# Kernel tuning notes

Hardware: AMD Instinct MI355X
Metric: run time of the kernel (lower is better)

## Reference

```python
import jax, jax.numpy as jnp
import numpy as np

DIM = 512
HEADS = 8
HEAD_DIM = 64
INNER = HEADS * HEAD_DIM  # 512
FF = DIM * 2
EPS = 1e-5


def layernorm(x, g, b):
    mu = jnp.mean(x, axis=-1, keepdims=True)
    var = jnp.var(x, axis=-1, keepdims=True)
    return (x - mu) * jax.lax.rsqrt(var + EPS) * g + b


def setup_inputs() -> dict:
    key = jax.random.key(0)
    ks = jax.random.split(key, 10)
    s = lambda fan_in: 1.0 / np.sqrt(fan_in)
    return {
        "x": jax.random.normal(ks[0], (4, 2048, DIM), dtype=jnp.float32),
        "ln1_g": jnp.ones((DIM,), jnp.float32),
        "ln1_b": jnp.zeros((DIM,), jnp.float32),
        "w_qkv": jax.random.normal(ks[1], (DIM, 3 * INNER), jnp.float32) * s(DIM),
        "w_out": jax.random.normal(ks[2], (INNER, DIM), jnp.float32) * s(INNER),
        "b_out": jnp.zeros((DIM,), jnp.float32),
        "ln2_g": jnp.ones((DIM,), jnp.float32),
        "ln2_b": jnp.zeros((DIM,), jnp.float32),
        "w1": jax.random.normal(ks[3], (DIM, FF), jnp.float32) * s(DIM),
        "b1": jnp.zeros((FF,), jnp.float32),
        "w2": jax.random.normal(ks[4], (FF, DIM), jnp.float32) * s(FF),
        "b2": jnp.zeros((DIM,), jnp.float32),
    }


def reference(x, ln1_g, ln1_b, w_qkv, w_out, b_out, ln2_g, ln2_b, w1, b1, w2, b2):
    b, n, _ = x.shape
    # --- pre-LN MHSA ---
    h = layernorm(x, ln1_g, ln1_b)
    qkv = h @ w_qkv  # [b, n, 3*inner]
    q, k, v = jnp.split(qkv, 3, axis=-1)
    to_heads = lambda t: t.reshape(b, n, HEADS, HEAD_DIM).transpose(0, 2, 1, 3)
    q, k, v = to_heads(q), to_heads(k), to_heads(v)
    scores = jnp.einsum('bhid,bhjd->bhij', q, k) * (HEAD_DIM ** -0.5)
    attn = jax.nn.softmax(scores, axis=-1)
    attended = jnp.einsum('bhij,bhjd->bhid', attn, v)
    attended = attended.transpose(0, 2, 1, 3).reshape(b, n, INNER)
    x = attended @ w_out + b_out + x
    # --- pre-LN MLP ---
    h = layernorm(x, ln2_g, ln2_b)
    h = jax.nn.gelu(h @ w1 + b1, approximate=False)
    x = h @ w2 + b2 + x
    return x
```

## Files before the change

kernel.cpp:

```cpp
#include <hip/hip_runtime.h>
#include <math.h>


#define TOKENS 8192
#define SEQ    2048
typedef unsigned short u16;
typedef __attribute__((ext_vector_type(8))) _Float16 h8;
typedef __attribute__((ext_vector_type(4))) float f32x4;
typedef __attribute__((ext_vector_type(4))) unsigned short u16x4;

#define BAR_V0 asm volatile("s_waitcnt vmcnt(0) lgkmcnt(0)\n\ts_barrier" ::: "memory")
#define BAR_V4 asm volatile("s_waitcnt vmcnt(4) lgkmcnt(0)\n\ts_barrier" ::: "memory")

__device__ __forceinline__ u16 f2h(float f) {
    _Float16 h = (_Float16)f;
    return __builtin_bit_cast(u16, h);
}
__device__ __forceinline__ void a16(void* lds, const void* g) {
    __builtin_amdgcn_global_load_lds(
        (const __attribute__((address_space(1))) unsigned int*)g,
        (__attribute__((address_space(3))) unsigned int*)lds, 16, 0, 0);
}
__device__ __forceinline__ float gelu_exact(float v) {
    return 0.5f * v * (1.0f + erff(v * 0.70710678118654752f));
}

__global__ __launch_bounds__(256) void prep_k(const float* __restrict__ wqkv,
                                              const float* __restrict__ wout,
                                              const float* __restrict__ w1,
                                              const float* __restrict__ w2,
                                              u16* __restrict__ dqkv,
                                              u16* __restrict__ dout,
                                              u16* __restrict__ d1,
                                              u16* __restrict__ d2,
                                              const float* __restrict__ x,
                                              const float* __restrict__ g,
                                              const float* __restrict__ bta,
                                              u16* __restrict__ oh) {
    const int tid = threadIdx.x;
    if (blockIdx.x >= 512) {
        const int lane = tid & 63;
        const int row  = ((blockIdx.x - 512) << 2) + (tid >> 6);
        const float* xr = x + ((size_t)row << 9) + (lane << 3);
        float v[8];
        *(float4*)&v[0] = *(const float4*)xr;
        *(float4*)&v[4] = *(const float4*)(xr + 4);
        float s = 0.f, ss = 0.f;
#pragma unroll
        for (int i = 0; i < 8; i++) { s += v[i]; ss += v[i] * v[i]; }
#pragma unroll
        for (int m = 32; m; m >>= 1) {
            s  += __shfl_xor(s, m, 64);
            ss += __shfl_xor(ss, m, 64);
        }
        const float mu   = s * (1.0f / 512.0f);
        const float rstd = rsqrtf(ss * (1.0f / 512.0f) - mu * mu + 1e-5f);
        float gg[8], bb[8];
        *(float4*)&gg[0] = *(const float4*)(g + (lane << 3));
        *(float4*)&gg[4] = *(const float4*)(g + (lane << 3) + 4);
        *(float4*)&bb[0] = *(const float4*)(bta + (lane << 3));
        *(float4*)&bb[4] = *(const float4*)(bta + (lane << 3) + 4);
        union { u16 us[8]; uint4 q; } H;
#pragma unroll
        for (int i = 0; i < 8; i++) H.us[i] = f2h((v[i] - mu) * rstd * gg[i] + bb[i]);
        *(uint4*)&oh[((size_t)row << 9) + (lane << 3)] = H.q;
        return;
    }
    __shared__ float t[64][65];
    int b = blockIdx.x;
    const float* src; u16* dst; int K, N, n0, k0;
    if (b < 192)      { src = wqkv; dst = dqkv; K = 512;  N = 1536; n0 = (b % 24) << 6; k0 = (b / 24) << 6; }
    else if (b < 256) { b -= 192; src = wout; dst = dout; K = 512;  N = 512;  n0 = (b & 7) << 6;  k0 = (b >> 3) << 6; }
    else if (b < 384) { b -= 256; src = w1;   dst = d1;   K = 512;  N = 1024; n0 = (b & 15) << 6; k0 = (b >> 4) << 6; }
    else              { b -= 384; src = w2;   dst = d2;   K = 1024; N = 512;  n0 = (b & 7) << 6;  k0 = (b >> 3) << 6; }
    {
        const int kr = tid >> 2, nc = (tid & 3) << 4;
        const float* p = src + (size_t)(k0 + kr) * N + n0 + nc;
#pragma unroll
        for (int i = 0; i < 4; i++)
            *(float4*)&t[kr][nc + (i << 2)] = *(const float4*)(p + (i << 2));
    }
    __syncthreads();
    {
        const int nr = tid >> 2, kc = (tid & 3) << 4;
        union { u16 us[16]; uint4 q[2]; } H;
#pragma unroll
        for (int i = 0; i < 16; i++) H.us[i] = f2h(t[kc + i][nr]);
        const size_t o = (size_t)(n0 + nr) * K + k0 + kc;
        *(uint4*)&dst[o] = H.q[0];
        *(uint4*)&dst[o + 8] = H.q[1];
    }
}

__global__ __launch_bounds__(256) void ln_k(const float* __restrict__ x,
                                            const float* __restrict__ g,
                                            const float* __restrict__ bta,
                                            u16* __restrict__ oh) {
    const int lane = threadIdx.x & 63;
    const int row  = (blockIdx.x << 2) + (threadIdx.x >> 6);
    const float* xr = x + ((size_t)row << 9) + (lane << 3);
    float v[8];
    *(float4*)&v[0] = *(const float4*)xr;
    *(float4*)&v[4] = *(const float4*)(xr + 4);
    float s = 0.f, ss = 0.f;
#pragma unroll
    for (int i = 0; i < 8; i++) { s += v[i]; ss += v[i] * v[i]; }
#pragma unroll
    for (int m = 32; m; m >>= 1) {
        s  += __shfl_xor(s, m, 64);
        ss += __shfl_xor(ss, m, 64);
    }
    const float mu   = s * (1.0f / 512.0f);
    const float rstd = rsqrtf(ss * (1.0f / 512.0f) - mu * mu + 1e-5f);
    float gg[8], bb[8];
    *(float4*)&gg[0] = *(const float4*)(g + (lane << 3));
    *(float4*)&gg[4] = *(const float4*)(g + (lane << 3) + 4);
    *(float4*)&bb[0] = *(const float4*)(bta + (lane << 3));
    *(float4*)&bb[4] = *(const float4*)(bta + (lane << 3) + 4);
    union { u16 us[8]; uint4 q; } H;
#pragma unroll
    for (int i = 0; i < 8; i++) H.us[i] = f2h((v[i] - mu) * rstd * gg[i] + bb[i]);
    *(uint4*)&oh[((size_t)row << 9) + (lane << 3)] = H.q;
}

template <int EPI>
__global__ __launch_bounds__(256, 3) void sgemm_k(
    const u16* __restrict__ A, const u16* __restrict__ B,
    const float* __restrict__ bias, const float* __restrict__ res,
    float* __restrict__ Cf, u16* __restrict__ Ch, u16* __restrict__ Dh,
    int M, int N, int K) {
    __shared__ u16 sm[16384];
    const int tid = threadIdx.x;
    const int lane = tid & 63, wv = tid >> 6;
    const int col = lane & 15, quad = lane >> 4;
    const int wm = (wv & 1) << 6, wn = (wv >> 1) << 6;
    const int bm = blockIdx.y << 7, bn = blockIdx.x << 7;

    const int r0 = tid >> 2,         c0 = (tid & 3) ^ ((r0 >> 1) & 3);
    const int r1 = (tid + 256) >> 2, c1 = (tid & 3) ^ ((r1 >> 1) & 3);
    const u16* Ag0 = A + (size_t)(bm + r0) * K + c0 * 8;
    const u16* Ag1 = A + (size_t)(bm + r1) * K + c1 * 8;
    const u16* Bg0 = B + (size_t)(bn + r0) * K + c0 * 8;
    const u16* Bg1 = B + (size_t)(bn + r1) * K + c1 * 8;
    const int lw0 = wv * 512, lw1 = wv * 512 + 2048;
    const int swz = (col >> 1) & 3;
    const f32x4 z4 = {0.f, 0.f, 0.f, 0.f};
    f32x4 acc[4][4] = {{z4,z4,z4,z4},{z4,z4,z4,z4},{z4,z4,z4,z4},{z4,z4,z4,z4}};

    a16(&sm[lw0],        Ag0);  a16(&sm[lw1],        Ag1);
    a16(&sm[lw0 + 4096], Bg0);  a16(&sm[lw1 + 4096], Bg1);

    int ib = 0;
    for (int k0 = 0; k0 < K; k0 += 32, ib ^= 1) {
        BAR_V0;
        if (k0 + 32 < K) {
            const int nb = (ib ^ 1) * 8192;
            const int kn = k0 + 32;
            a16(&sm[nb + lw0],        Ag0 + kn);  a16(&sm[nb + lw1],        Ag1 + kn);
            a16(&sm[nb + lw0 + 4096], Bg0 + kn);  a16(&sm[nb + lw1 + 4096], Bg1 + kn);
        }
        const int cb = ib * 8192;
        h8 af[4];
#pragma unroll
        for (int mt = 0; mt < 4; mt++) {
            const int ra = cb + (wm + (mt << 4) + col) * 32 + ((quad ^ swz) << 3);
            af[mt] = *(const h8*)&sm[ra];
        }
#pragma unroll
        for (int nt = 0; nt < 4; nt++) {
            const int rb = cb + 4096 + (wn + (nt << 4) + col) * 32 + ((quad ^ swz) << 3);
            h8 bf = *(const h8*)&sm[rb];
#pragma unroll
            for (int mt = 0; mt < 4; mt++)
                acc[mt][nt] = __builtin_amdgcn_mfma_f32_16x16x32_f16(af[mt], bf, acc[mt][nt], 0, 0, 0);
        }
    }

    if constexpr (EPI == 0) {
        if (bn >= 1024) {
            const int hd0  = (bn - 1024) >> 6;
            const int b8   = (bm >> 11) << 3;
            const int keyb = bm & 2047;
            __syncthreads();
#pragma unroll
            for (int hf = 0; hf < 2; hf++) {
                if ((wv >> 1) == hf) {
#pragma unroll
                    for (int mt = 0; mt < 4; mt++)
#pragma unroll
                    for (int rr = 0; rr < 4; rr++) {
                        const int key = wm + (mt << 4) + (quad << 2) + rr;
#pragma unroll
                        for (int nt = 0; nt < 4; nt++) {
                            const int dl = (nt << 4) + col;
                            sm[dl * 136 + key] = f2h(acc[mt][nt][rr]);
                        }
                    }
                }
                __syncthreads();
                {
                    const int d = tid >> 2;
#pragma unroll
                    for (int c = 0; c < 4; c++) {
                        const int key0 = ((((tid & 3) << 2) + c) << 3);
                        const size_t gb = ((size_t)(b8 + hd0 + hf) << 17)
                                        + ((size_t)d << 11) + keyb + key0;
                        *(uint4*)&Dh[gb] = *(const uint4*)&sm[d * 136 + key0];
                    }
                }
                __syncthreads();
            }
            return;
        }
    }

    float bs[4];
    if constexpr (EPI >= 1) {
#pragma unroll
        for (int nt = 0; nt < 4; nt++) bs[nt] = bias[bn + wn + (nt << 4) + col];
    }
#pragma unroll
    for (int mt = 0; mt < 4; mt++) {
#pragma unroll
        for (int rr = 0; rr < 4; rr++) {
            const int row = bm + wm + (mt << 4) + (quad << 2) + rr;
#pragma unroll
            for (int nt = 0; nt < 4; nt++) {
                const int colg = bn + wn + (nt << 4) + col;
                float v = acc[mt][nt][rr];
                if constexpr (EPI == 0) {
                    const int b = row >> 11, key = row & 2047;
                    if (bn < 512) {
                        Cf[((size_t)row << 9) + colg] = v;
                    } else {
                        const int hd = (colg - 512) >> 6, d = colg & 63;
                        Ch[((size_t)((b << 3) + hd) << 17) + (key << 6) + d] = f2h(v);
                    }
                } else if constexpr (EPI == 2) {
                    Ch[(size_t)row * N + colg] = f2h(gelu_exact(v + bs[nt]));
                } else {
                    const size_t o = (size_t)row * N + colg;
                    Cf[o] = v + bs[nt] + res[o];
                }
            }
        }
    }
}

__global__ __launch_bounds__(128, 2) void attn_k(const float* __restrict__ q,
                                                 const u16* __restrict__ kh,
                                                 const u16* __restrict__ vth,
                                                 u16* __restrict__ ah) {
    __shared__ u16 sm[16384];
    const int tid = threadIdx.x;
    const int lane = tid & 63, wv = tid >> 6;
    const int col = lane & 15, quad = lane >> 4;
    const int qt = blockIdx.x, bh = blockIdx.y;
    const int b = bh >> 3, h = bh & 7;
    const size_t tok0 = (size_t)b * SEQ;
    const size_t bhK = (size_t)bh << 17;
    const int q0 = qt << 6;

    h8 qf[2][2];
#pragma unroll
    for (int sub = 0; sub < 2; sub++) {
        const int qrow = q0 + (wv << 5) + (sub << 4) + col;
        const float* qp = q + ((tok0 + qrow) << 9) + (h << 6) + (quad << 3);
#pragma unroll
        for (int kc = 0; kc < 2; kc++) {
            float v[8];
            *(float4*)&v[0] = *(const float4*)(qp + (kc << 5));
            *(float4*)&v[4] = *(const float4*)(qp + (kc << 5) + 4);
            union { u16 us[8]; h8 v8; } H;
#pragma unroll
            for (int i = 0; i < 8; i++) H.us[i] = f2h(v[i] * 0.125f);
            qf[sub][kc] = H.v8;
        }
    }

    const f32x4 z4 = {0.f, 0.f, 0.f, 0.f};
    f32x4 o[2][4] = {{z4, z4, z4, z4}, {z4, z4, z4, z4}};
    float m_run[2] = {-1e30f, -1e30f}, l_run[2] = {0.f, 0.f};

    size_t kbz[4], vbz[4];
    int doff[4];
#pragma unroll
    for (int j = 0; j < 4; j++) {
        const int C = (((j << 1) + wv) << 6) + lane;
        const int sr = C >> 3, sp = (C & 7) ^ (sr & 7);
        kbz[j] = bhK + ((size_t)sr << 6) + (sp << 3);
        vbz[j] = bhK + ((size_t)sr << 11) + (sp << 3);
        doff[j] = (((j << 1) + wv) << 9);
    }

#pragma unroll
    for (int j = 0; j < 4; j++) a16(&sm[doff[j]], kh + kbz[j]);

    int ib = 0;
    for (int jt = 0; jt < 32; jt++, ib ^= 1) {
        BAR_V0;
        {
            const size_t vo = (size_t)jt << 6;
#pragma unroll
            for (int j = 0; j < 4; j++) a16(&sm[8192 + doff[j]], vth + vbz[j] + vo);
            const size_t kon = (size_t)((jt + 1) & 31) << 12;
            const int nb = (ib ^ 1) << 12;
#pragma unroll
            for (int j = 0; j < 4; j++) a16(&sm[nb + doff[j]], kh + kbz[j] + kon);
        }

        const int cb = ib << 12;
        f32x4 st0[4] = {z4, z4, z4, z4}, st1[4] = {z4, z4, z4, z4};
#pragma unroll
        for (int kb = 0; kb < 4; kb++) {
            const int key = (kb << 4) + col;
            const int r64 = key << 6, k7 = key & 7;
#pragma unroll
            for (int kc = 0; kc < 2; kc++) {
                const int ofs = cb + r64 + ((((kc << 2) + quad) ^ k7) << 3);
                h8 kf = *(const h8*)&sm[ofs];
                st0[kb] = __builtin_amdgcn_mfma_f32_16x16x32_f16(kf, qf[0][kc], st0[kb], 0, 0, 0);
                st1[kb] = __builtin_amdgcn_mfma_f32_16x16x32_f16(kf, qf[1][kc], st1[kb], 0, 0, 0);
            }
        }

#pragma unroll
        for (int sub = 0; sub < 2; sub++) {
            f32x4* st = sub ? st1 : st0;
            float mx = st[0][0];
#pragma unroll
            for (int kb = 0; kb < 4; kb++)
#pragma unroll
                for (int r = 0; r < 4; r++) mx = fmaxf(mx, st[kb][r]);
            mx = fmaxf(mx, __shfl_xor(mx, 16));
            mx = fmaxf(mx, __shfl_xor(mx, 32));
            const float mn = fmaxf(m_run[sub], mx);
            const float alp = __expf(m_run[sub] - mn);
            m_run[sub] = mn;
            float p[16];
            float rs = 0.0f;
#pragma unroll
            for (int kb = 0; kb < 4; kb++)
#pragma unroll
                for (int r = 0; r < 4; r++) {
                    float e = __expf(st[kb][r] - mn);
                    p[(kb << 2) + r] = e;
                    rs += e;
                }
            rs += __shfl_xor(rs, 16);
            rs += __shfl_xor(rs, 32);
            l_run[sub] = l_run[sub] * alp + rs;
            float aO[4];
#pragma unroll
            for (int r = 0; r < 4; r++) aO[r] = __shfl(alp, (quad << 2) + r);
#pragma unroll
            for (int db = 0; db < 4; db++) {
                o[sub][db][0] *= aO[0]; o[sub][db][1] *= aO[1];
                o[sub][db][2] *= aO[2]; o[sub][db][3] *= aO[3];
            }
            const int prow = (wv << 5) + (sub << 4) + col;
            const int p64 = prow << 6, p7 = prow & 7;
#pragma unroll
            for (int kb = 0; kb < 4; kb++) {
                u16x4 hv;
#pragma unroll
                for (int r = 0; r < 4; r++) hv[r] = f2h(p[(kb << 2) + r]);
                const int c = (kb << 1) + (quad >> 1);
                *(u16x4*)&sm[12288 + p64 + ((c ^ p7) << 3) + ((quad & 1) << 2)] = hv;
            }
        }

        BAR_V4;

        h8 pf[2][2];
#pragma unroll
        for (int sub = 0; sub < 2; sub++) {
            const int prow = (wv << 5) + (sub << 4) + col;
            const int p64 = prow << 6, p7 = prow & 7;
#pragma unroll
            for (int kc = 0; kc < 2; kc++)
                pf[sub][kc] = *(const h8*)&sm[12288 + p64 + ((((kc << 2) + quad) ^ p7) << 3)];
        }
#pragma unroll
        for (int db = 0; db < 4; db++) {
            const int d = (db << 4) + col;
            const int v64 = 8192 + (d << 6), d7 = d & 7;
#pragma unroll
            for (int kc = 0; kc < 2; kc++) {
                h8 vf = *(const h8*)&sm[v64 + ((((kc << 2) + quad) ^ d7) << 3)];
                o[0][db] = __builtin_amdgcn_mfma_f32_16x16x32_f16(pf[0][kc], vf, o[0][db], 0, 0, 0);
                o[1][db] = __builtin_amdgcn_mfma_f32_16x16x32_f16(pf[1][kc], vf, o[1][db], 0, 0, 0);
            }
        }
    }

#pragma unroll
    for (int sub = 0; sub < 2; sub++) {
        float linv[4];
#pragma unroll
        for (int r = 0; r < 4; r++) linv[r] = 1.0f / __shfl(l_run[sub], (quad << 2) + r);
#pragma unroll
        for (int r = 0; r < 4; r++) {
            const size_t rowo = ((tok0 + q0 + (wv << 5) + (sub << 4) + (quad << 2) + r) << 9)
                                + (h << 6) + col;
#pragma unroll
            for (int db = 0; db < 4; db++)
                ah[rowo + (db << 4)] = f2h(o[sub][db][r] * linv[r]);
        }
    }
}

extern "C" void kernel_launch(void* const* d_in, const int* in_sizes, int n_in,
                              void* d_out, int out_size, void* d_ws, size_t ws_size,
                              hipStream_t stream) {
    const float* x     = (const float*)d_in[0];
    const float* ln1_g = (const float*)d_in[1];
    const float* ln1_b = (const float*)d_in[2];
    const float* w_qkv = (const float*)d_in[3];
    const float* w_out = (const float*)d_in[4];
    const float* b_out = (const float*)d_in[5];
    const float* ln2_g = (const float*)d_in[6];
    const float* ln2_b = (const float*)d_in[7];
    const float* w1    = (const float*)d_in[8];
    const float* b1    = (const float*)d_in[9];
    const float* w2    = (const float*)d_in[10];
    const float* b2    = (const float*)d_in[11];
    float* out = (float*)d_out;

    u16* wqkvh = (u16*)d_ws;
    u16* wouth = wqkvh + 1536 * 512;
    u16* w1h   = wouth + 512 * 512;
    u16* w2h   = w1h + 1024 * 512;
    u16* hbuf  = w2h + 512 * 1024;
    float* qbuf = (float*)(hbuf + (size_t)TOKENS * 512);
    float* x2   = qbuf;
    u16* kh  = (u16*)(qbuf + (size_t)TOKENS * 512);
    u16* vth = kh + (size_t)32 * 131072;
    u16* gh  = kh;

    prep_k<<<2560, 256, 0, stream>>>(w_qkv, w_out, w1, w2, wqkvh, wouth, w1h, w2h,
                                     x, ln1_g, ln1_b, hbuf);
    sgemm_k<0><<<dim3(12, 64), 256, 0, stream>>>(hbuf, wqkvh, nullptr, nullptr,
                                                 qbuf, kh, vth, TOKENS, 1536, 512);
    attn_k<<<dim3(32, 32), 128, 0, stream>>>(qbuf, kh, vth, hbuf);
    sgemm_k<1><<<dim3(4, 64), 256, 0, stream>>>(hbuf, wouth, b_out, x,
                                                x2, nullptr, nullptr, TOKENS, 512, 512);
    ln_k<<<TOKENS / 4, 256, 0, stream>>>(x2, ln2_g, ln2_b, hbuf);
    sgemm_k<2><<<dim3(8, 64), 256, 0, stream>>>(hbuf, w1h, b1, nullptr,
                                                nullptr, gh, nullptr, TOKENS, 1024, 512);
    sgemm_k<3><<<dim3(4, 64), 256, 0, stream>>>(gh, w2h, b2, x2,
                                                out, nullptr, nullptr, TOKENS, 512, 1024);
}
```

Measured before the change: 254.1 us.

## Double-buffer V tiles and prefetch K two tiles ahead in attention

The attention kernel now double-buffers the V tile as well as K, growing LDS from 32 KB to 40 KB. K is prefetched two iterations ahead and V one iteration ahead, so the loop no longer drains all loads at the top-of-loop barrier. This is meant to hide global-load latency behind the QK and PV MFMA work. It also raises wave priority around the MFMA blocks with s_setprio, and the vmcnt bookkeeping becomes more delicate, which risks a race if the load counts are wrong.

```diff
diff --git a/kernel.cpp b/kernel.cpp
--- a/kernel.cpp
+++ b/kernel.cpp
@@ -10,7 +10,6 @@
 typedef __attribute__((ext_vector_type(4))) unsigned short u16x4;
 
 #define BAR_V0 asm volatile("s_waitcnt vmcnt(0) lgkmcnt(0)\n\ts_barrier" ::: "memory")
-#define BAR_V4 asm volatile("s_waitcnt vmcnt(4) lgkmcnt(0)\n\ts_barrier" ::: "memory")
 
 __device__ __forceinline__ u16 f2h(float f) {
     _Float16 h = (_Float16)f;
@@ -251,7 +250,7 @@
                                                  const u16* __restrict__ kh,
                                                  const u16* __restrict__ vth,
                                                  u16* __restrict__ ah) {
-    __shared__ u16 sm[16384];
+    __shared__ u16 sm[20480];
     const int tid = threadIdx.x;
     const int lane = tid & 63, wv = tid >> 6;
     const int col = lane & 15, quad = lane >> 4;
@@ -295,22 +294,28 @@
 
 #pragma unroll
     for (int j = 0; j < 4; j++) a16(&sm[doff[j]], kh + kbz[j]);
+#pragma unroll
+    for (int j = 0; j < 4; j++) a16(&sm[8192 + doff[j]], vth + vbz[j]);
+#pragma unroll
+    for (int j = 0; j < 4; j++) a16(&sm[4096 + doff[j]], kh + kbz[j] + 4096);
 
     int ib = 0;
     for (int jt = 0; jt < 32; jt++, ib ^= 1) {
-        BAR_V0;
-        {
-            const size_t vo = (size_t)jt << 6;
-#pragma unroll
-            for (int j = 0; j < 4; j++) a16(&sm[8192 + doff[j]], vth + vbz[j] + vo);
-            const size_t kon = (size_t)((jt + 1) & 31) << 12;
-            const int nb = (ib ^ 1) << 12;
-#pragma unroll
-            for (int j = 0; j < 4; j++) a16(&sm[nb + doff[j]], kh + kbz[j] + kon);
+        if (jt < 31) {
+            asm volatile("s_waitcnt vmcnt(4) lgkmcnt(0)\n\ts_barrier" ::: "memory");
+        } else {
+            asm volatile("s_waitcnt vmcnt(0) lgkmcnt(0)\n\ts_barrier" ::: "memory");
+        }
+        if (jt < 31) {
+            const size_t vo = (size_t)(jt + 1) << 6;
+            const int vb = 8192 + ((ib ^ 1) << 12);
+#pragma unroll
+            for (int j = 0; j < 4; j++) a16(&sm[vb + doff[j]], vth + vbz[j] + vo);
         }
 
         const int cb = ib << 12;
         f32x4 st0[4] = {z4, z4, z4, z4}, st1[4] = {z4, z4, z4, z4};
+        __builtin_amdgcn_s_setprio(1);
 #pragma unroll
         for (int kb = 0; kb < 4; kb++) {
             const int key = (kb << 4) + col;
@@ -323,6 +328,7 @@
                 st1[kb] = __builtin_amdgcn_mfma_f32_16x16x32_f16(kf, qf[1][kc], st1[kb], 0, 0, 0);
             }
         }
+        __builtin_amdgcn_s_setprio(0);
 
 #pragma unroll
         for (int sub = 0; sub < 2; sub++) {
@@ -366,11 +372,18 @@
 #pragma unroll
                 for (int r = 0; r < 4; r++) hv[r] = f2h(p[(kb << 2) + r]);
                 const int c = (kb << 1) + (quad >> 1);
-                *(u16x4*)&sm[12288 + p64 + ((c ^ p7) << 3) + ((quad & 1) << 2)] = hv;
-            }
-        }
-
-        BAR_V4;
+                *(u16x4*)&sm[16384 + p64 + ((c ^ p7) << 3) + ((quad & 1) << 2)] = hv;
+            }
+        }
+
+        asm volatile("s_waitcnt lgkmcnt(0)\n\ts_barrier" ::: "memory");
+
+        if (jt < 30) {
+            const size_t ko = (size_t)(jt + 2) << 12;
+            const int kb2 = ib << 12;
+#pragma unroll
+            for (int j = 0; j < 4; j++) a16(&sm[kb2 + doff[j]], kh + kbz[j] + ko);
+        }
 
         h8 pf[2][2];
 #pragma unroll
@@ -379,12 +392,14 @@
             const int p64 = prow << 6, p7 = prow & 7;
 #pragma unroll
             for (int kc = 0; kc < 2; kc++)
-                pf[sub][kc] = *(const h8*)&sm[12288 + p64 + ((((kc << 2) + quad) ^ p7) << 3)];
-        }
+                pf[sub][kc] = *(const h8*)&sm[16384 + p64 + ((((kc << 2) + quad) ^ p7) << 3)];
+        }
+        const int vbase = 8192 + (ib << 12);
+        __builtin_amdgcn_s_setprio(1);
 #pragma unroll
         for (int db = 0; db < 4; db++) {
             const int d = (db << 4) + col;
-            const int v64 = 8192 + (d << 6), d7 = d & 7;
+            const int v64 = vbase + (d << 6), d7 = d & 7;
 #pragma unroll
             for (int kc = 0; kc < 2; kc++) {
                 h8 vf = *(const h8*)&sm[v64 + ((((kc << 2) + quad) ^ d7) << 3)];
@@ -392,6 +407,7 @@
                 o[1][db] = __builtin_amdgcn_mfma_f32_16x16x32_f16(pf[1][kc], vf, o[1][db], 0, 0, 0);
             }
         }
+        __builtin_amdgcn_s_setprio(0);
     }
 
 #pragma unroll
```

New measurement: 248.4 us. 1.02x faster.
